# Kernel tuning notes

Measured on AMD Instinct MI355X. Metric: run time of the kernel, lower is better.

## Reference

```python
import jax, jax.numpy as jnp
import numpy as np

N = 8192
E = 262144
F_IN, H1, H2 = 512, 256, 128


def setup_inputs() -> dict:
    key = jax.random.key(0)
    ks = jax.random.split(key, 7)
    x = jax.random.normal(ks[0], (N, F_IN), dtype=jnp.float32)
    # glorot-ish init scale
    W1 = jax.random.normal(ks[1], (F_IN, H1), dtype=jnp.float32) * (1.0 / np.sqrt(F_IN))
    W2 = jax.random.normal(ks[2], (H1, H2), dtype=jnp.float32) * (1.0 / np.sqrt(H1))
    W3 = jax.random.normal(ks[3], (H1, H2), dtype=jnp.float32) * (1.0 / np.sqrt(H1))
    edge_w = jax.random.uniform(ks[4], (E,), dtype=jnp.float32) / 32.0  # ~normalized adj
    row = jax.random.randint(ks[5], (E,), 0, N, dtype=jnp.int64)
    col = jax.random.randint(ks[6], (E,), 0, N, dtype=jnp.int64)
    return {"x": x, "W1": W1, "W2": W2, "W3": W3, "edge_w": edge_w, "row": row, "col": col}


def _spmm(row, col, edge_w, h):
    # sparse adjacency aggregate: out[i] = sum_{e: row[e]==i} edge_w[e] * h[col[e]]
    msgs = edge_w[:, None] * h[col]  # [E, d]
    return jax.ops.segment_sum(msgs, row, num_segments=N)


def reference(x, W1, W2, W3, edge_w, row, col):
    # gc1: dropout(off, eval) -> matmul -> spmm -> relu
    h1 = jax.nn.relu(_spmm(row, col, edge_w, x @ W1))  # [N, H1]
    # gc2 / gc3: identity activation
    mu = _spmm(row, col, edge_w, h1 @ W2)              # [N, H2]
    logvar = _spmm(row, col, edge_w, h1 @ W3)          # [N, H2]
    z = mu  # eval-mode reparameterize returns mu
    adj_rec = z @ z.T  # [N, N], decoder act = identity
    return (h1, adj_rec, mu, logvar, z)
```

## Files before the change

kernel.cpp:

```cpp
#include <hip/hip_runtime.h>

typedef __bf16 bf16_t;
typedef __bf16 bf16x4 __attribute__((ext_vector_type(4)));
typedef __bf16 bf16x8 __attribute__((ext_vector_type(8)));
typedef float floatx4 __attribute__((ext_vector_type(4)));

static constexpr int NN  = 8192;
static constexpr int FIN = 512;
static constexpr int NH1 = 256;
static constexpr int NH2 = 128;
static constexpr int NE  = 262144;
static constexpr int CAP = 128;

static constexpr size_t OFF_H1     = 0;
static constexpr size_t OFF_ADJ    = (size_t)NN * NH1;
static constexpr size_t OFF_MU     = OFF_ADJ + (size_t)NN * NN;
static constexpr size_t OFF_LOGVAR = OFF_MU + (size_t)NN * NH2;
static constexpr size_t OFF_Z      = OFF_LOGVAR + (size_t)NN * NH2;

template <int KD, int RT, bool ABF, int EPI>
__device__ __forceinline__ void gemm_body(
    int bx, int by, const float* __restrict__ Af, const bf16_t* __restrict__ Abf,
    const bf16_t* __restrict__ BT, float* __restrict__ C, int ldc,
    bf16_t* __restrict__ zb, int ldz, float* __restrict__ L, int lane, int wid) {
  const int l15 = lane & 15;
  const int lg  = lane >> 4;
  const int brow = by * (RT * 32) + (wid >> 1) * (RT * 16);
  const int bcol = bx * 128 + (wid & 1) * 64;

  floatx4 acc[RT][4];
#pragma unroll
  for (int i = 0; i < RT; ++i)
#pragma unroll
    for (int j = 0; j < 4; ++j) acc[i][j] = (floatx4){0.f, 0.f, 0.f, 0.f};

#pragma unroll 1
  for (int kk = 0; kk < KD; kk += 32) {
    bf16x8 a[RT], b[4];
#pragma unroll
    for (int rt = 0; rt < RT; ++rt) {
      const int r = brow + rt * 16 + l15;
      if constexpr (ABF) {
        a[rt] = *(const bf16x8*)(Abf + (size_t)r * KD + kk + lg * 8);
      } else {
        const float* p = Af + (size_t)r * KD + kk + lg * 8;
        const floatx4 lo = *(const floatx4*)p;
        const floatx4 hi = *(const floatx4*)(p + 4);
        bf16x8 t;
        t[0] = (bf16_t)lo[0]; t[1] = (bf16_t)lo[1];
        t[2] = (bf16_t)lo[2]; t[3] = (bf16_t)lo[3];
        t[4] = (bf16_t)hi[0]; t[5] = (bf16_t)hi[1];
        t[6] = (bf16_t)hi[2]; t[7] = (bf16_t)hi[3];
        a[rt] = t;
      }
    }
#pragma unroll
    for (int ct = 0; ct < 4; ++ct) {
      const int c = bcol + ct * 16 + l15;
      b[ct] = *(const bf16x8*)(BT + (size_t)c * KD + kk + lg * 8);
    }
#pragma unroll
    for (int rt = 0; rt < RT; ++rt)
#pragma unroll
      for (int ct = 0; ct < 4; ++ct)
        acc[rt][ct] = __builtin_amdgcn_mfma_f32_16x16x32_bf16(
            a[rt], b[ct], acc[rt][ct], 0, 0, 0);
  }

#pragma unroll
  for (int rt = 0; rt < RT; ++rt) {
#pragma unroll
    for (int ct = 0; ct < 4; ++ct)
#pragma unroll
      for (int r = 0; r < 4; ++r)
        L[(lg * 4 + r) * 68 + ct * 16 + l15] = acc[rt][ct][r];
    __builtin_amdgcn_wave_barrier();
#pragma unroll
    for (int it = 0; it < 4; ++it) {
      const int idx = it * 64 + lane;
      const int rr = idx >> 4, c4 = idx & 15;
      const floatx4 v = *(const floatx4*)(L + rr * 68 + c4 * 4);
      const int orow = brow + rt * 16 + rr;
      const int gc = bcol + c4 * 4;
      if constexpr (EPI == 0) {
        __builtin_nontemporal_store(v, (floatx4*)(C + (size_t)orow * ldc + gc));
      } else {
        bf16x4 o;
        o[0] = (bf16_t)v[0]; o[1] = (bf16_t)v[1];
        o[2] = (bf16_t)v[2]; o[3] = (bf16_t)v[3];
        *(bf16x4*)(zb + (size_t)orow * ldz + gc) = o;
      }
    }
    __builtin_amdgcn_wave_barrier();
  }
}

__global__ __launch_bounds__(256) void k_prep(
    const float* __restrict__ W1, const float* __restrict__ W2,
    const float* __restrict__ W3, bf16_t* __restrict__ W1T,
    bf16_t* __restrict__ W23T, int* __restrict__ counts) {
  const int gid = blockIdx.x * 256 + threadIdx.x;
  if (gid <= NN) counts[gid] = 0;
  if (gid < NH1 * FIN) {
    const int n = gid >> 9, k = gid & 511;
    W1T[gid] = (bf16_t)W1[k * NH1 + n];
  }
  if (gid < NH1 * NH1) {
    const int n = gid >> 8, k = gid & 255;
    W23T[gid] = (bf16_t)(n < NH2 ? W2[k * NH2 + n] : W3[k * NH2 + (n - NH2)]);
  }
}

__global__ __launch_bounds__(256) void k_fat(
    const float* __restrict__ x, const bf16_t* __restrict__ W1T,
    bf16_t* __restrict__ XWb, const int* __restrict__ row,
    const int* __restrict__ col, const float* __restrict__ edge_w,
    int* __restrict__ counts, uint2* __restrict__ bucket,
    uint4* __restrict__ spill) {
  __shared__ float lt[4][16 * 68];
  const int bid = blockIdx.x;
  if (bid < 256) {
    const int lane = threadIdx.x & 63;
    const int wid  = threadIdx.x >> 6;
    gemm_body<FIN, 2, false, 2>(bid & 1, bid >> 1, x, nullptr, W1T, nullptr, 0,
                                XWb, NH1, lt[wid], lane, wid);
  } else {
    const int e = (bid - 256) * 256 + threadIdx.x;
    const int r = row[e];
    const int p = atomicAdd(&counts[r], 1);
    if (p < CAP) {
      uint2 v;
      v.x = (unsigned)col[e];
      v.y = __float_as_uint(edge_w[e]);
      bucket[(size_t)r * CAP + p] = v;
    } else {
      const int s = atomicAdd(&counts[NN], 1);
      uint4 v;
      v.x = (unsigned)r; v.y = (unsigned)col[e];
      v.z = __float_as_uint(edge_w[e]); v.w = 0;
      spill[s] = v;
    }
  }
}

__device__ __forceinline__ void spmm_gather_row(
    int r, int deg, const uint2* __restrict__ bucket,
    const uint4* __restrict__ spill, int ns, const bf16_t* __restrict__ src,
    int lane, int li, int g, float* __restrict__ acc) {
#pragma unroll
  for (int c = 0; c < 16; ++c) acc[c] = 0.f;
  for (int base = 0; base < deg; base += 64) {
    const int t = base + lane;
    uint2 cw;
    cw.x = 0; cw.y = 0;
    if (t < deg) cw = bucket[(size_t)r * CAP + t];
    const int cnt = min(64, deg - base);
#pragma unroll 2
    for (int j4 = 0; j4 < cnt; j4 += 4) {
      const int cj = __shfl((int)cw.x, j4 + g);
      const float wj = __shfl(__uint_as_float(cw.y), j4 + g);
      const bf16_t* p = src + (size_t)cj * NH1 + li * 16;
      const bf16x8 v0 = *(const bf16x8*)p;
      const bf16x8 v1 = *(const bf16x8*)(p + 8);
#pragma unroll
      for (int c = 0; c < 8; ++c) {
        acc[c]     += wj * (float)v0[c];
        acc[8 + c] += wj * (float)v1[c];
      }
    }
  }
  if (ns > 0 && g == 0) {
    for (int i = 0; i < ns; ++i) {
      const uint4 s = spill[i];
      if ((int)s.x == r) {
        const float wj = __uint_as_float(s.z);
        const bf16_t* p = src + (size_t)s.y * NH1 + li * 16;
        const bf16x8 v0 = *(const bf16x8*)p;
        const bf16x8 v1 = *(const bf16x8*)(p + 8);
#pragma unroll
        for (int c = 0; c < 8; ++c) {
          acc[c]     += wj * (float)v0[c];
          acc[8 + c] += wj * (float)v1[c];
        }
      }
    }
  }
}

__global__ __launch_bounds__(256) void spmm_bucket_relu(
    const int* __restrict__ counts, const uint2* __restrict__ bucket,
    const uint4* __restrict__ spill, const bf16_t* __restrict__ src,
    float* __restrict__ dst_f, bf16_t* __restrict__ dst_b) {
  const int lane = threadIdx.x & 63;
  const int r = blockIdx.x * 4 + (threadIdx.x >> 6);
  const int li = lane & 15;
  const int g  = lane >> 4;
  const int deg = min(counts[r], CAP);
  float acc[16];
  spmm_gather_row(r, deg, bucket, spill, counts[NN], src, lane, li, g, acc);
#pragma unroll
  for (int c = 0; c < 16; ++c) {
    acc[c] += __shfl_xor(acc[c], 16);
    acc[c] += __shfl_xor(acc[c], 32);
    acc[c] = fmaxf(acc[c], 0.f);
  }
  float o0, o1, o2, o3;
  switch (g) {
    case 0:  o0 = acc[0];  o1 = acc[1];  o2 = acc[2];  o3 = acc[3];  break;
    case 1:  o0 = acc[4];  o1 = acc[5];  o2 = acc[6];  o3 = acc[7];  break;
    case 2:  o0 = acc[8];  o1 = acc[9];  o2 = acc[10]; o3 = acc[11]; break;
    default: o0 = acc[12]; o1 = acc[13]; o2 = acc[14]; o3 = acc[15]; break;
  }
  const int ch = li * 16 + g * 4;
  floatx4 o = (floatx4){o0, o1, o2, o3};
  __builtin_nontemporal_store(o, (floatx4*)(dst_f + (size_t)r * NH1 + ch));
  bf16x4 ob;
  ob[0] = (bf16_t)o0; ob[1] = (bf16_t)o1; ob[2] = (bf16_t)o2; ob[3] = (bf16_t)o3;
  *(bf16x4*)(dst_b + (size_t)r * NH1 + ch) = ob;
}

__global__ __launch_bounds__(1024) void k_fuse23(
    const int* __restrict__ counts, const uint2* __restrict__ bucket,
    const uint4* __restrict__ spill, const bf16_t* __restrict__ h1b,
    const bf16_t* __restrict__ W23T, float* __restrict__ dout,
    bf16_t* __restrict__ zbf) {
  __shared__ bf16_t Lg[16][264];
  const int lane = threadIdx.x & 63;
  const int wid  = threadIdx.x >> 6;
  const int li = lane & 15;
  const int g  = lane >> 4;
  const int l15 = li;
  const int lg  = g;
  const int r0 = blockIdx.x * 16;
  const int r  = r0 + wid;

  const int deg = min(counts[r], CAP);
  float acc[16];
  spmm_gather_row(r, deg, bucket, spill, counts[NN], h1b, lane, li, g, acc);
#pragma unroll
  for (int c = 0; c < 16; ++c) {
    acc[c] += __shfl_xor(acc[c], 16);
    acc[c] += __shfl_xor(acc[c], 32);
  }
  float o0, o1, o2, o3;
  switch (g) {
    case 0:  o0 = acc[0];  o1 = acc[1];  o2 = acc[2];  o3 = acc[3];  break;
    case 1:  o0 = acc[4];  o1 = acc[5];  o2 = acc[6];  o3 = acc[7];  break;
    case 2:  o0 = acc[8];  o1 = acc[9];  o2 = acc[10]; o3 = acc[11]; break;
    default: o0 = acc[12]; o1 = acc[13]; o2 = acc[14]; o3 = acc[15]; break;
  }
  bf16x4 gv;
  gv[0] = (bf16_t)o0; gv[1] = (bf16_t)o1; gv[2] = (bf16_t)o2; gv[3] = (bf16_t)o3;
  *(bf16x4*)(&Lg[wid][li * 16 + g * 4]) = gv;
  __syncthreads();

  const int wc = wid * 16;
  floatx4 a2 = (floatx4){0.f, 0.f, 0.f, 0.f};
#pragma unroll
  for (int kk = 0; kk < NH1; kk += 32) {
    const bf16x8 af = *(const bf16x8*)(&Lg[l15][kk + lg * 8]);
    const bf16x8 bw =
        *(const bf16x8*)(W23T + (size_t)(wc + l15) * NH1 + kk + lg * 8);
    a2 = __builtin_amdgcn_mfma_f32_16x16x32_bf16(bw, af, a2, 0, 0, 0);
  }
  const int orow = r0 + l15;
  const int oc = wc + lg * 4;
  if (oc < NH2) {
    __builtin_nontemporal_store(a2,
                                (floatx4*)(dout + OFF_MU + (size_t)orow * NH2 + oc));
    __builtin_nontemporal_store(a2,
                                (floatx4*)(dout + OFF_Z + (size_t)orow * NH2 + oc));
    bf16x4 ob;
    ob[0] = (bf16_t)a2[0]; ob[1] = (bf16_t)a2[1];
    ob[2] = (bf16_t)a2[2]; ob[3] = (bf16_t)a2[3];
    *(bf16x4*)(zbf + (size_t)orow * NH2 + oc) = ob;
  } else {
    __builtin_nontemporal_store(
        a2, (floatx4*)(dout + OFF_LOGVAR + (size_t)orow * NH2 + oc - NH2));
  }
}

template <int KD, int RT, bool ABF, int EPI, bool SWZ>
__global__ __launch_bounds__(256) void mfma_gemm(
    const float* __restrict__ Af, const bf16_t* __restrict__ Abf,
    const bf16_t* __restrict__ BT, float* __restrict__ C, int ldc,
    bf16_t* __restrict__ zb, int ldz) {
  __shared__ float lt[4][16 * 68];
  int bx, by;
  if constexpr (SWZ) {
    const int bid = blockIdx.x;
    const int s = (bid & 7) * 512 + (bid >> 3);
    by = s >> 6; bx = s & 63;
  } else {
    bx = blockIdx.x; by = blockIdx.y;
  }
  const int lane = threadIdx.x & 63;
  const int wid  = threadIdx.x >> 6;
  gemm_body<KD, RT, ABF, EPI>(bx, by, Af, Abf, BT, C, ldc, zb, ldz, lt[wid],
                              lane, wid);
}

extern "C" void kernel_launch(void* const* d_in, const int* in_sizes, int n_in,
                              void* d_out, int out_size, void* d_ws, size_t ws_size,
                              hipStream_t stream) {
  const float* x      = (const float*)d_in[0];
  const float* W1     = (const float*)d_in[1];
  const float* W2     = (const float*)d_in[2];
  const float* W3     = (const float*)d_in[3];
  const float* edge_w = (const float*)d_in[4];
  const int*   row    = (const int*)d_in[5];
  const int*   col    = (const int*)d_in[6];
  float* out = (float*)d_out;
  char*  ws  = (char*)d_ws;

  bf16_t* XWb  = (bf16_t*)(ws);
  bf16_t* h1b  = (bf16_t*)(ws + (4u << 20));
  bf16_t* W1T  = (bf16_t*)(ws + (8u << 20));
  bf16_t* W23T = (bf16_t*)(ws + (8u << 20) + (1u << 18));
  int*    counts = (int*)(ws + (8u << 20) + (3u << 18));
  uint2*  bucket = (uint2*)(ws + (9u << 20));
  uint4*  spill  = (uint4*)(ws + (17u << 20));
  bf16_t* zbf  = (bf16_t*)(ws + (17u << 20) + (1u << 16));

  k_prep<<<512, 256, 0, stream>>>(W1, W2, W3, W1T, W23T, counts);
  k_fat<<<1280, 256, 0, stream>>>(x, W1T, XWb, row, col, edge_w, counts, bucket,
                                  spill);
  spmm_bucket_relu<<<NN / 4, 256, 0, stream>>>(counts, bucket, spill, XWb,
                                               out + OFF_H1, h1b);
  k_fuse23<<<NN / 16, 1024, 0, stream>>>(counts, bucket, spill, h1b, W23T, out,
                                         zbf);
  mfma_gemm<NH2, 4, true, 0, true><<<4096, 256, 0, stream>>>(
      nullptr, zbf, zbf, out + OFF_ADJ, NN, nullptr, 0);
}
```

Measured before the change: 138.9 us.

## Replace tiled adj GEMM with persistent slab kernel keeping A rows in registers

The z@z.T output GEMM now runs as a dedicated kernel with 512 blocks. Each block owns 64 rows and a 2048-column slab, and each wave walks 512 columns. The A fragments are loaded once into registers and reused across all column tiles, and each B tile is loaded once per 16 columns. This removes the per-tile reload of A and cuts the tile launch count, which matters because the kernel is dominated by the 256MB output write. The cost is a larger per-wave LDS staging buffer (64x68 floats) and fewer blocks, which may lower occupancy.

```diff
diff --git a/kernel.cpp b/kernel.cpp
--- a/kernel.cpp
+++ b/kernel.cpp
@@ -82,14 +82,10 @@
       const floatx4 v = *(const floatx4*)(L + rr * 68 + c4 * 4);
       const int orow = brow + rt * 16 + rr;
       const int gc = bcol + c4 * 4;
-      if constexpr (EPI == 0) {
-        __builtin_nontemporal_store(v, (floatx4*)(C + (size_t)orow * ldc + gc));
-      } else {
-        bf16x4 o;
-        o[0] = (bf16_t)v[0]; o[1] = (bf16_t)v[1];
-        o[2] = (bf16_t)v[2]; o[3] = (bf16_t)v[3];
-        *(bf16x4*)(zb + (size_t)orow * ldz + gc) = o;
-      }
+      bf16x4 o;
+      o[0] = (bf16_t)v[0]; o[1] = (bf16_t)v[1];
+      o[2] = (bf16_t)v[2]; o[3] = (bf16_t)v[3];
+      *(bf16x4*)(zb + (size_t)orow * ldz + gc) = o;
     }
     __builtin_amdgcn_wave_barrier();
   }
@@ -280,24 +276,60 @@
   }
 }
 
-template <int KD, int RT, bool ABF, int EPI, bool SWZ>
-__global__ __launch_bounds__(256) void mfma_gemm(
-    const float* __restrict__ Af, const bf16_t* __restrict__ Abf,
-    const bf16_t* __restrict__ BT, float* __restrict__ C, int ldc,
-    bf16_t* __restrict__ zb, int ldz) {
-  __shared__ float lt[4][16 * 68];
-  int bx, by;
-  if constexpr (SWZ) {
-    const int bid = blockIdx.x;
-    const int s = (bid & 7) * 512 + (bid >> 3);
-    by = s >> 6; bx = s & 63;
-  } else {
-    bx = blockIdx.x; by = blockIdx.y;
-  }
+__global__ __launch_bounds__(256) void adj_slab(
+    const bf16_t* __restrict__ zb, float* __restrict__ C) {
+  __shared__ float lt[4][64 * 68];
+  const int bid = blockIdx.x;
+  const int s = (bid & 7) * 64 + (bid >> 3);
+  const int rp = s >> 2, cs = s & 3;
   const int lane = threadIdx.x & 63;
   const int wid  = threadIdx.x >> 6;
-  gemm_body<KD, RT, ABF, EPI>(bx, by, Af, Abf, BT, C, ldc, zb, ldz, lt[wid],
-                              lane, wid);
+  const int l15 = lane & 15;
+  const int lg  = lane >> 4;
+  const int r0 = rp * 64;
+  const int c0 = cs * 2048 + wid * 512;
+  float* L = lt[wid];
+
+  bf16x8 a_[4][4];
+#pragma unroll
+  for (int rt = 0; rt < 4; ++rt)
+#pragma unroll
+    for (int ks = 0; ks < 4; ++ks)
+      a_[rt][ks] = *(const bf16x8*)(zb + (size_t)(r0 + rt * 16 + l15) * NH2 +
+                                    ks * 32 + lg * 8);
+
+#pragma unroll 1
+  for (int ctg = 0; ctg < 8; ++ctg) {
+    const int cgbase = c0 + ctg * 64;
+#pragma unroll
+    for (int ctm = 0; ctm < 4; ++ctm) {
+      const int c = cgbase + ctm * 16 + l15;
+      bf16x8 b_[4];
+#pragma unroll
+      for (int ks = 0; ks < 4; ++ks)
+        b_[ks] = *(const bf16x8*)(zb + (size_t)c * NH2 + ks * 32 + lg * 8);
+#pragma unroll
+      for (int rt = 0; rt < 4; ++rt) {
+        floatx4 acc = (floatx4){0.f, 0.f, 0.f, 0.f};
+#pragma unroll
+        for (int ks = 0; ks < 4; ++ks)
+          acc = __builtin_amdgcn_mfma_f32_16x16x32_bf16(a_[rt][ks], b_[ks], acc,
+                                                        0, 0, 0);
+#pragma unroll
+        for (int r = 0; r < 4; ++r)
+          L[(rt * 16 + lg * 4 + r) * 68 + ctm * 16 + l15] = acc[r];
+      }
+    }
+    __builtin_amdgcn_wave_barrier();
+#pragma unroll
+    for (int it = 0; it < 16; ++it) {
+      const int rr = it * 4 + lg;
+      const floatx4 v = *(const floatx4*)(L + rr * 68 + l15 * 4);
+      __builtin_nontemporal_store(
+          v, (floatx4*)(C + (size_t)(r0 + rr) * NN + cgbase + l15 * 4));
+    }
+    __builtin_amdgcn_wave_barrier();
+  }
 }
 
 extern "C" void kernel_launch(void* const* d_in, const int* in_sizes, int n_in,
@@ -329,6 +361,5 @@
                                                out + OFF_H1, h1b);
   k_fuse23<<<NN / 16, 1024, 0, stream>>>(counts, bucket, spill, h1b, W23T, out,
                                          zbf);
-  mfma_gemm<NH2, 4, true, 0, true><<<4096, 256, 0, stream>>>(
-      nullptr, zbf, zbf, out + OFF_ADJ, NN, nullptr, 0);
-}
+  adj_slab<<<512, 256, 0, stream>>>(zbf, out + OFF_ADJ);
+}
```

Result: faster. 127.9 us (-7.9%).
